# Performance work log

Hardware: AMD Instinct MI355X
Metric: run time of the kernel (lower is better)

Reference implementation:

```python
import jax, jax.numpy as jnp
import numpy as np

N = 100000
E = 3200000
EMBED = 64
RBF = 16
EPS_ANGLE = 1e-8
EPS_NORM = 1e-12  # F.normalize default eps


def _linear(h, W, b):
    return h @ W + b


def setup_inputs() -> dict:
    key = jax.random.key(0)
    ks = jax.random.split(key, 12)
    s = lambda fan_in: 1.0 / np.sqrt(fan_in)
    return {
        "x": jax.random.normal(ks[0], (N, EMBED), jnp.float32),
        "coord": jax.random.normal(ks[1], (N, 3), jnp.float32),
        "rbf_feature": jax.random.normal(ks[2], (E, RBF), jnp.float32),
        "edge_index": jax.random.randint(ks[3], (2, E), 0, N, jnp.int64),
        # edge_mlp: Linear(RBF+1, EMBED) -> SiLU -> Linear(EMBED, EMBED)
        "W1": jax.random.uniform(ks[4], (RBF + 1, EMBED), jnp.float32, -s(RBF + 1), s(RBF + 1)),
        "b1": jnp.zeros((EMBED,), jnp.float32),
        "W2": jax.random.uniform(ks[5], (EMBED, EMBED), jnp.float32, -s(EMBED), s(EMBED)),
        "b2": jnp.zeros((EMBED,), jnp.float32),
        # update_mlp: Linear(EMBED, EMBED) -> SiLU -> Linear(EMBED, EMBED)
        "W3": jax.random.uniform(ks[6], (EMBED, EMBED), jnp.float32, -s(EMBED), s(EMBED)),
        "b3": jnp.zeros((EMBED,), jnp.float32),
        "W4": jax.random.uniform(ks[7], (EMBED, EMBED), jnp.float32, -s(EMBED), s(EMBED)),
        "b4": jnp.zeros((EMBED,), jnp.float32),
    }


def reference(x, coord, rbf_feature, edge_index, W1, b1, W2, b2, W3, b3, W4, b4):
    row, col = edge_index[0], edge_index[1]
    # gather per-edge displacement vectors: [E, 3]
    v = coord[row] - coord[col]
    # compute_angle(v, -v): normalize both, cosine, clamp, acos
    norm = jnp.maximum(jnp.linalg.norm(v, axis=-1, keepdims=True), EPS_NORM)
    vn = v / norm
    cos_angle = jnp.clip(jnp.sum(vn * (-vn), axis=-1), -1.0 + EPS_ANGLE, 1.0 - EPS_ANGLE)
    angle = jnp.arccos(cos_angle)[:, None]  # [E, 1]
    edge_feat = jnp.concatenate([rbf_feature, angle], axis=-1)  # [E, RBF+1]
    # edge MLP
    edge_msg = _linear(jax.nn.silu(_linear(edge_feat, W1, b1)), W2, b2)  # [E, EMBED]
    # scatter-add to source nodes (index_add_ over row)
    agg = jax.ops.segment_sum(edge_msg, row, num_segments=x.shape[0])  # [N, EMBED]
    # node update
    return x + _linear(jax.nn.silu(_linear(agg, W3, b3)), W4, b4)
```

## Files before the change

### kernel.cpp

```cpp
#include <hip/hip_runtime.h>
#include <hip/hip_fp16.h>
#include <hip/hip_bf16.h>

typedef __attribute__((ext_vector_type(8))) short bf16x8;
typedef __attribute__((ext_vector_type(4))) float f32x4;

constexpr int EMBED = 64;
constexpr int RBF   = 16;

__device__ __forceinline__ short f2bf(float f) {
    __hip_bfloat16 h = __float2bfloat16(f);
    return *reinterpret_cast<short*>(&h);
}
__device__ __forceinline__ unsigned pk_bf(float lo, float hi) {
    unsigned l = (unsigned short)f2bf(lo);
    unsigned h = (unsigned short)f2bf(hi);
    return l | (h << 16);
}
__device__ __forceinline__ unsigned pk_f16(float lo, float hi) {
    __half2 h = __halves2half2(__float2half_rn(lo), __float2half_rn(hi));
    return *reinterpret_cast<unsigned*>(&h);
}
__device__ __forceinline__ void atom_pk_add_f16(__half* addr, unsigned data) {
    asm volatile("global_atomic_pk_add_f16 %0, %1, off"
                 :: "v"(addr), "v"(data) : "memory");
}
__device__ __forceinline__ float silu(float x) {
    return x * __builtin_amdgcn_rcpf(1.0f + __expf(-x));
}
__device__ __forceinline__ int ch_map(int t, int c) {
    return (t & 1) + 2 * c + 32 * (t >> 1);
}

constexpr short BF16_PI  = (short)0x4049;
constexpr short BF16_PI2 = (short)0x3FC9;

template <bool GUARD, bool F16>
__global__ __launch_bounds__(256, 2) void edge_kernel(
    const float* __restrict__ rbf,
    const int* __restrict__ ei,
    const float* __restrict__ W1,
    const float* __restrict__ b1,
    const float* __restrict__ W2,
    const float* __restrict__ b2,
    void* __restrict__ agg,
    int e_base, int E)
{
    __shared__ __align__(16) short lds_s[4][16 * 64];
    __shared__ int lds_row[256];

    const int tid  = threadIdx.x;
    const int lane = tid & 63;
    const int wave = tid >> 6;
    const int g = lane >> 4;
    const int c = lane & 15;
    const int blk_e0 = e_base + blockIdx.x * 256;

    {
        const int e = blk_e0 + tid;
        lds_row[tid] = (!GUARD || e < E) ? ei[e] : 0;
    }
    __syncthreads();

    bf16x8 b1f[4];
    float b1v[4], b2v[4];
#pragma unroll
    for (int t = 0; t < 4; ++t) {
        const int ch = ch_map(t, c);
#pragma unroll
        for (int j = 0; j < 8; ++j) {
            const int k = g * 8 + j;
            b1f[t][j] = (k <= RBF) ? f2bf(W1[k * EMBED + ch]) : (short)0;
        }
        b1v[t] = b1[ch];
        b2v[t] = b2[ch];
    }
    bf16x8 b2f[2][4];
#pragma unroll
    for (int kk = 0; kk < 2; ++kk)
#pragma unroll
        for (int t = 0; t < 4; ++t) {
            const int ch = ch_map(t, c);
#pragma unroll
            for (int j = 0; j < 8; ++j)
                b2f[kk][t][j] = f2bf(W2[(kk * 32 + g * 8 + j) * EMBED + ch]);
        }

    char* const sl = reinterpret_cast<char*>(lds_s[wave]);
    const int e0w = blk_e0 + wave * 64;

#pragma unroll 1
    for (int mt = 0; mt < 4; ++mt) {
        const int e0 = e0w + mt * 16;
        if (GUARD && e0 >= E) break;
        const int el0 = wave * 64 + mt * 16;

        bf16x8 a = {};
        const int ea = e0 + c;
        const bool ev = !GUARD || (ea < E);
        if (g < 2) {
            if (ev) {
                const float4 p0 = *reinterpret_cast<const float4*>(rbf + (long long)ea * RBF + g * 8);
                const float4 p1 = *reinterpret_cast<const float4*>(rbf + (long long)ea * RBF + g * 8 + 4);
                a[0] = f2bf(p0.x); a[1] = f2bf(p0.y); a[2] = f2bf(p0.z); a[3] = f2bf(p0.w);
                a[4] = f2bf(p1.x); a[5] = f2bf(p1.y); a[6] = f2bf(p1.z); a[7] = f2bf(p1.w);
            }
        } else if (g == 2 && ev) {
            const int row = lds_row[el0 + c];
            const int col = ei[E + ea];
            a[0] = (row == col) ? BF16_PI2 : BF16_PI;
        }

        f32x4 acc1[4];
#pragma unroll
        for (int t = 0; t < 4; ++t) {
            f32x4 ci = {b1v[t], b1v[t], b1v[t], b1v[t]};
            acc1[t] = __builtin_amdgcn_mfma_f32_16x16x32_bf16(a, b1f[t], ci, 0, 0, 0);
        }

#pragma unroll
        for (int r = 0; r < 4; ++r) {
            const int erow = g * 4 + r;
            const int swz = (erow & 7) << 4;
            *reinterpret_cast<unsigned*>(sl + erow * 128 + ((4 * c) ^ swz)) =
                pk_bf(silu(acc1[0][r]), silu(acc1[1][r]));
            *reinterpret_cast<unsigned*>(sl + erow * 128 + ((64 + 4 * c) ^ swz)) =
                pk_bf(silu(acc1[2][r]), silu(acc1[3][r]));
        }
        __builtin_amdgcn_wave_barrier();

        bf16x8 a2[2];
#pragma unroll
        for (int kk = 0; kk < 2; ++kk) {
            const int byte = c * 128 + ((kk * 64 + g * 16) ^ ((c & 7) << 4));
            a2[kk] = *reinterpret_cast<const bf16x8*>(sl + byte);
        }
        __builtin_amdgcn_wave_barrier();

        f32x4 acc2[4];
#pragma unroll
        for (int t = 0; t < 4; ++t) {
            f32x4 ci = {b2v[t], b2v[t], b2v[t], b2v[t]};
            acc2[t] = __builtin_amdgcn_mfma_f32_16x16x32_bf16(a2[0], b2f[0][t], ci, 0, 0, 0);
            acc2[t] = __builtin_amdgcn_mfma_f32_16x16x32_bf16(a2[1], b2f[1][t], acc2[t], 0, 0, 0);
        }

#pragma unroll
        for (int r = 0; r < 4; ++r) {
            const int eat = e0 + g * 4 + r;
            if (!GUARD || eat < E) {
                const unsigned row = (unsigned)lds_row[el0 + g * 4 + r];
                if (F16) {
                    __half* const dst = reinterpret_cast<__half*>(agg) + row * 64u;
                    atom_pk_add_f16(dst + 2 * c,      pk_f16(acc2[0][r], acc2[1][r]));
                    atom_pk_add_f16(dst + 32 + 2 * c, pk_f16(acc2[2][r], acc2[3][r]));
                } else {
                    float* const dst = reinterpret_cast<float*>(agg) + row * 64u;
                    atomicAdd(dst + 2 * c,      acc2[0][r]);
                    atomicAdd(dst + 2 * c + 1,  acc2[1][r]);
                    atomicAdd(dst + 32 + 2 * c, acc2[2][r]);
                    atomicAdd(dst + 33 + 2 * c, acc2[3][r]);
                }
            }
        }
    }
}

template <bool F16>
__global__ __launch_bounds__(256) void node_kernel(
    const float* __restrict__ x, const void* __restrict__ aggv,
    const float* __restrict__ W3, const float* __restrict__ b3,
    const float* __restrict__ W4, const float* __restrict__ b4,
    float* __restrict__ out, int nn)
{
    __shared__ __align__(16) float lds_s[4][EMBED];
    const int lane = threadIdx.x & 63;
    const int wave = threadIdx.x >> 6;
    float w3c[EMBED], w4c[EMBED];
#pragma unroll
    for (int j = 0; j < EMBED; ++j) w3c[j] = W3[j * EMBED + lane];
#pragma unroll
    for (int j = 0; j < EMBED; ++j) w4c[j] = W4[j * EMBED + lane];
    const float b3v = b3[lane];
    const float b4v = b4[lane];
    const float4* s4 = reinterpret_cast<const float4*>(lds_s[wave]);
    const int wid = blockIdx.x * 4 + wave;
    const int nw  = gridDim.x * 4;
    for (int n = wid; n < nn; n += nw) {
        const long long base = (long long)n * EMBED + lane;
        float a;
        if (F16) a = __half2float(reinterpret_cast<const __half*>(aggv)[base]);
        else     a = reinterpret_cast<const float*>(aggv)[base];
        lds_s[wave][lane] = a;
        __builtin_amdgcn_wave_barrier();
        float acc = b3v;
#pragma unroll
        for (int j4 = 0; j4 < EMBED / 4; ++j4) {
            const float4 sv = s4[j4];
            acc = fmaf(sv.x, w3c[4 * j4 + 0], acc);
            acc = fmaf(sv.y, w3c[4 * j4 + 1], acc);
            acc = fmaf(sv.z, w3c[4 * j4 + 2], acc);
            acc = fmaf(sv.w, w3c[4 * j4 + 3], acc);
        }
        const float s = acc * __builtin_amdgcn_rcpf(1.0f + __expf(-acc));
        __builtin_amdgcn_wave_barrier();
        lds_s[wave][lane] = s;
        __builtin_amdgcn_wave_barrier();
        float acc2 = b4v;
#pragma unroll
        for (int j4 = 0; j4 < EMBED / 4; ++j4) {
            const float4 sv = s4[j4];
            acc2 = fmaf(sv.x, w4c[4 * j4 + 0], acc2);
            acc2 = fmaf(sv.y, w4c[4 * j4 + 1], acc2);
            acc2 = fmaf(sv.z, w4c[4 * j4 + 2], acc2);
            acc2 = fmaf(sv.w, w4c[4 * j4 + 3], acc2);
        }
        __builtin_amdgcn_wave_barrier();
        out[base] = x[base] + acc2;
    }
}

extern "C" void kernel_launch(void* const* d_in, const int* in_sizes, int n_in,
                              void* d_out, int out_size, void* d_ws, size_t ws_size,
                              hipStream_t stream) {
    const float* x      = (const float*)d_in[0];
    const float* rbf    = (const float*)d_in[2];
    const int*   ei     = (const int*)d_in[3];
    const float* W1 = (const float*)d_in[4];
    const float* b1 = (const float*)d_in[5];
    const float* W2 = (const float*)d_in[6];
    const float* b2 = (const float*)d_in[7];
    const float* W3 = (const float*)d_in[8];
    const float* b3 = (const float*)d_in[9];
    const float* W4 = (const float*)d_in[10];
    const float* b4 = (const float*)d_in[11];
    float* out = (float*)d_out;

    const int E  = (int)(in_sizes[3] / 2);
    const int nn = in_sizes[0] / EMBED;

    void* agg16 = d_ws;
    const size_t neededF16 = (size_t)nn * EMBED * sizeof(__half);

    const int nfull = E / 256;
    const int rem   = E - nfull * 256;

    if (ws_size >= neededF16) {
        hipMemsetAsync(agg16, 0, neededF16, stream);
        if (nfull)
            edge_kernel<false, true><<<dim3(nfull), dim3(256), 0, stream>>>(
                rbf, ei, W1, b1, W2, b2, agg16, 0, E);
        if (rem)
            edge_kernel<true, true><<<dim3(1), dim3(256), 0, stream>>>(
                rbf, ei, W1, b1, W2, b2, agg16, nfull * 256, E);
        node_kernel<true><<<dim3(2048), dim3(256), 0, stream>>>(
            x, agg16, W3, b3, W4, b4, out, nn);
    } else {
        hipMemsetAsync(out, 0, (size_t)nn * EMBED * sizeof(float), stream);
        if (nfull)
            edge_kernel<false, false><<<dim3(nfull), dim3(256), 0, stream>>>(
                rbf, ei, W1, b1, W2, b2, out, 0, E);
        if (rem)
            edge_kernel<true, false><<<dim3(1), dim3(256), 0, stream>>>(
                rbf, ei, W1, b1, W2, b2, out, nfull * 256, E);
        node_kernel<false><<<dim3(2048), dim3(256), 0, stream>>>(
            x, out, W3, b3, W4, b4, out, nn);
    }
}
```

Measured before the change: 428.2 us.

## Move second edge-MLP linear layer after scatter using linearity and degree-scaled bias

Because the second edge linear layer is linear, the edge kernel now scatter-adds silu(first layer) per source node and counts node degree, and a new per-node kernel applies W2 plus degree times b2. This removes the second MFMA stage and its LDS round trip from the per-edge path, leaving the same amount of atomic traffic. It adds a degree atomic per edge, an extra node kernel, and an extra fp32 agg buffer in workspace. If the workspace is too small, execution falls back to the original fused path.

Result: slower. 589.8 us (+37.7%).

```diff
diff --git a/kernel.cpp b/kernel.cpp
--- a/kernel.cpp
+++ b/kernel.cpp
@@ -35,33 +35,209 @@
 constexpr short BF16_PI  = (short)0x4049;
 constexpr short BF16_PI2 = (short)0x3FC9;
 
-template <bool GUARD, bool F16>
-__global__ __launch_bounds__(256, 2) void edge_kernel(
+template <bool GUARD>
+__global__ __launch_bounds__(256, 2) void edge_sum_kernel(
+    const float* __restrict__ rbf,
+    const int* __restrict__ ei,
+    const float* __restrict__ W1,
+    const float* __restrict__ b1,
+    __half* __restrict__ ssum,
+    float* __restrict__ deg,
+    int e_base, int E)
+{
+    __shared__ int lds_row[256];
+
+    const int tid  = threadIdx.x;
+    const int lane = tid & 63;
+    const int wave = tid >> 6;
+    const int g = lane >> 4;
+    const int c = lane & 15;
+    const int blk_e0 = e_base + blockIdx.x * 256;
+
+    {
+        const int e = blk_e0 + tid;
+        const bool v = !GUARD || (e < E);
+        const int row = v ? ei[e] : 0;
+        lds_row[tid] = row;
+        if (v) atomicAdd(&deg[row], 1.0f);
+    }
+    __syncthreads();
+
+    bf16x8 b1f[4];
+    float b1v[4];
+#pragma unroll
+    for (int t = 0; t < 4; ++t) {
+        const int ch = ch_map(t, c);
+#pragma unroll
+        for (int j = 0; j < 8; ++j) {
+            const int k = g * 8 + j;
+            b1f[t][j] = (k <= RBF) ? f2bf(W1[k * EMBED + ch]) : (short)0;
+        }
+        b1v[t] = b1[ch];
+    }
+
+    const int e0w = blk_e0 + wave * 64;
+
+    bf16x8 a1[4];
+#pragma unroll
+    for (int mt = 0; mt < 4; ++mt) {
+        bf16x8 a = {};
+        const int e0 = e0w + mt * 16;
+        const int ea = e0 + c;
+        const bool ev = !GUARD || (ea < E);
+        if (g < 2) {
+            if (ev) {
+                const float4 p0 = *reinterpret_cast<const float4*>(rbf + (long long)ea * RBF + g * 8);
+                const float4 p1 = *reinterpret_cast<const float4*>(rbf + (long long)ea * RBF + g * 8 + 4);
+                a[0] = f2bf(p0.x); a[1] = f2bf(p0.y); a[2] = f2bf(p0.z); a[3] = f2bf(p0.w);
+                a[4] = f2bf(p1.x); a[5] = f2bf(p1.y); a[6] = f2bf(p1.z); a[7] = f2bf(p1.w);
+            }
+        } else if (g == 2 && ev) {
+            const int row = lds_row[wave * 64 + mt * 16 + c];
+            const int col = ei[E + ea];
+            a[0] = (row == col) ? BF16_PI2 : BF16_PI;
+        }
+        a1[mt] = a;
+    }
+
+#pragma unroll
+    for (int mt = 0; mt < 4; ++mt) {
+        const int e0 = e0w + mt * 16;
+        if (GUARD && e0 >= E) break;
+        const int el0 = wave * 64 + mt * 16;
+
+        f32x4 s[4];
+#pragma unroll
+        for (int t = 0; t < 4; ++t) {
+            f32x4 ci = {b1v[t], b1v[t], b1v[t], b1v[t]};
+            s[t] = __builtin_amdgcn_mfma_f32_16x16x32_bf16(a1[mt], b1f[t], ci, 0, 0, 0);
+        }
+
+#pragma unroll
+        for (int r = 0; r < 4; ++r) {
+            const int eat = e0 + g * 4 + r;
+            if (!GUARD || eat < E) {
+                const unsigned row = (unsigned)lds_row[el0 + g * 4 + r];
+                __half* const dst = ssum + row * 64u;
+                atom_pk_add_f16(dst + 2 * c,
+                                pk_f16(silu(s[0][r]), silu(s[1][r])));
+                atom_pk_add_f16(dst + 32 + 2 * c,
+                                pk_f16(silu(s[2][r]), silu(s[3][r])));
+            }
+        }
+    }
+}
+
+__global__ __launch_bounds__(256) void k_agg(
+    const __half* __restrict__ ssum, const float* __restrict__ deg,
+    const float* __restrict__ W2, const float* __restrict__ b2,
+    float* __restrict__ agg, int nn)
+{
+    __shared__ __align__(16) float lds_s[4][EMBED];
+    const int lane = threadIdx.x & 63;
+    const int wave = threadIdx.x >> 6;
+
+    float w2c[EMBED];
+#pragma unroll
+    for (int j = 0; j < EMBED; ++j) w2c[j] = W2[j * EMBED + lane];
+    const float b2v = b2[lane];
+
+    const float4* s4 = reinterpret_cast<const float4*>(lds_s[wave]);
+    const int wid = blockIdx.x * 4 + wave;
+    const int nw  = gridDim.x * 4;
+    for (int n = wid; n < nn; n += nw) {
+        const long long base = (long long)n * EMBED + lane;
+        const float a = __half2float(ssum[base]);
+
+        lds_s[wave][lane] = a;
+        __builtin_amdgcn_wave_barrier();
+
+        float acc = deg[n] * b2v;
+#pragma unroll
+        for (int j4 = 0; j4 < EMBED / 4; ++j4) {
+            const float4 sv = s4[j4];
+            acc = fmaf(sv.x, w2c[4 * j4 + 0], acc);
+            acc = fmaf(sv.y, w2c[4 * j4 + 1], acc);
+            acc = fmaf(sv.z, w2c[4 * j4 + 2], acc);
+            acc = fmaf(sv.w, w2c[4 * j4 + 3], acc);
+        }
+        __builtin_amdgcn_wave_barrier();
+
+        agg[base] = acc;
+    }
+}
+
+__global__ __launch_bounds__(256) void node_kernel(
+    const float* __restrict__ x, const float* __restrict__ aggv,
+    const float* __restrict__ W3, const float* __restrict__ b3,
+    const float* __restrict__ W4, const float* __restrict__ b4,
+    float* __restrict__ out, int nn)
+{
+    __shared__ __align__(16) float lds_s[4][EMBED];
+    const int lane = threadIdx.x & 63;
+    const int wave = threadIdx.x >> 6;
+    float w3c[EMBED], w4c[EMBED];
+#pragma unroll
+    for (int j = 0; j < EMBED; ++j) w3c[j] = W3[j * EMBED + lane];
+#pragma unroll
+    for (int j = 0; j < EMBED; ++j) w4c[j] = W4[j * EMBED + lane];
+    const float b3v = b3[lane];
+    const float b4v = b4[lane];
+    const float4* s4 = reinterpret_cast<const float4*>(lds_s[wave]);
+    const int wid = blockIdx.x * 4 + wave;
+    const int nw  = gridDim.x * 4;
+    for (int n = wid; n < nn; n += nw) {
+        const long long base = (long long)n * EMBED + lane;
+        const float a = aggv[base];
+        lds_s[wave][lane] = a;
+        __builtin_amdgcn_wave_barrier();
+        float acc = b3v;
+#pragma unroll
+        for (int j4 = 0; j4 < EMBED / 4; ++j4) {
+            const float4 sv = s4[j4];
+            acc = fmaf(sv.x, w3c[4 * j4 + 0], acc);
+            acc = fmaf(sv.y, w3c[4 * j4 + 1], acc);
+            acc = fmaf(sv.z, w3c[4 * j4 + 2], acc);
+            acc = fmaf(sv.w, w3c[4 * j4 + 3], acc);
+        }
+        const float s = acc * __builtin_amdgcn_rcpf(1.0f + __expf(-acc));
+        __builtin_amdgcn_wave_barrier();
+        lds_s[wave][lane] = s;
+        __builtin_amdgcn_wave_barrier();
+        float acc2 = b4v;
+#pragma unroll
+        for (int j4 = 0; j4 < EMBED / 4; ++j4) {
+            const float4 sv = s4[j4];
+            acc2 = fmaf(sv.x, w4c[4 * j4 + 0], acc2);
+            acc2 = fmaf(sv.y, w4c[4 * j4 + 1], acc2);
+            acc2 = fmaf(sv.z, w4c[4 * j4 + 2], acc2);
+            acc2 = fmaf(sv.w, w4c[4 * j4 + 3], acc2);
+        }
+        __builtin_amdgcn_wave_barrier();
+        out[base] = x[base] + acc2;
+    }
+}
+
+__global__ __launch_bounds__(256, 2) void edge_kernel_fb(
     const float* __restrict__ rbf,
     const int* __restrict__ ei,
     const float* __restrict__ W1,
     const float* __restrict__ b1,
     const float* __restrict__ W2,
     const float* __restrict__ b2,
-    void* __restrict__ agg,
-    int e_base, int E)
+    float* __restrict__ agg,
+    int E)
 {
     __shared__ __align__(16) short lds_s[4][16 * 64];
     __shared__ int lds_row[256];
-
-    const int tid  = threadIdx.x;
-    const int lane = tid & 63;
-    const int wave = tid >> 6;
-    const int g = lane >> 4;
-    const int c = lane & 15;
-    const int blk_e0 = e_base + blockIdx.x * 256;
-
+    const int tid = threadIdx.x, lane = tid & 63, wave = tid >> 6;
+    const int g = lane >> 4, c = lane & 15;
+    const int blk_e0 = blockIdx.x * 256;
     {
         const int e = blk_e0 + tid;
-        lds_row[tid] = (!GUARD || e < E) ? ei[e] : 0;
+        lds_row[tid] = (e < E) ? ei[e] : 0;
     }
     __syncthreads();
-
     bf16x8 b1f[4];
     float b1v[4], b2v[4];
 #pragma unroll
@@ -85,19 +261,16 @@
             for (int j = 0; j < 8; ++j)
                 b2f[kk][t][j] = f2bf(W2[(kk * 32 + g * 8 + j) * EMBED + ch]);
         }
-
     char* const sl = reinterpret_cast<char*>(lds_s[wave]);
     const int e0w = blk_e0 + wave * 64;
-
 #pragma unroll 1
     for (int mt = 0; mt < 4; ++mt) {
         const int e0 = e0w + mt * 16;
-        if (GUARD && e0 >= E) break;
+        if (e0 >= E) break;
         const int el0 = wave * 64 + mt * 16;
-
         bf16x8 a = {};
         const int ea = e0 + c;
-        const bool ev = !GUARD || (ea < E);
+        const bool ev = (ea < E);
         if (g < 2) {
             if (ev) {
                 const float4 p0 = *reinterpret_cast<const float4*>(rbf + (long long)ea * RBF + g * 8);
@@ -110,14 +283,12 @@
             const int col = ei[E + ea];
             a[0] = (row == col) ? BF16_PI2 : BF16_PI;
         }
-
         f32x4 acc1[4];
 #pragma unroll
         for (int t = 0; t < 4; ++t) {
             f32x4 ci = {b1v[t], b1v[t], b1v[t], b1v[t]};
             acc1[t] = __builtin_amdgcn_mfma_f32_16x16x32_bf16(a, b1f[t], ci, 0, 0, 0);
         }
-
 #pragma unroll
         for (int r = 0; r < 4; ++r) {
             const int erow = g * 4 + r;
@@ -128,7 +299,6 @@
                 pk_bf(silu(acc1[2][r]), silu(acc1[3][r]));
         }
         __builtin_amdgcn_wave_barrier();
-
         bf16x8 a2[2];
 #pragma unroll
         for (int kk = 0; kk < 2; ++kk) {
@@ -136,7 +306,6 @@
             a2[kk] = *reinterpret_cast<const bf16x8*>(sl + byte);
         }
         __builtin_amdgcn_wave_barrier();
-
         f32x4 acc2[4];
 #pragma unroll
         for (int t = 0; t < 4; ++t) {
@@ -144,79 +313,19 @@
             acc2[t] = __builtin_amdgcn_mfma_f32_16x16x32_bf16(a2[0], b2f[0][t], ci, 0, 0, 0);
             acc2[t] = __builtin_amdgcn_mfma_f32_16x16x32_bf16(a2[1], b2f[1][t], acc2[t], 0, 0, 0);
         }
-
 #pragma unroll
         for (int r = 0; r < 4; ++r) {
             const int eat = e0 + g * 4 + r;
-            if (!GUARD || eat < E) {
+            if (eat < E) {
                 const unsigned row = (unsigned)lds_row[el0 + g * 4 + r];
-                if (F16) {
-                    __half* const dst = reinterpret_cast<__half*>(agg) + row * 64u;
-                    atom_pk_add_f16(dst + 2 * c,      pk_f16(acc2[0][r], acc2[1][r]));
-                    atom_pk_add_f16(dst + 32 + 2 * c, pk_f16(acc2[2][r], acc2[3][r]));
-                } else {
-                    float* const dst = reinterpret_cast<float*>(agg) + row * 64u;
-                    atomicAdd(dst + 2 * c,      acc2[0][r]);
-                    atomicAdd(dst + 2 * c + 1,  acc2[1][r]);
-                    atomicAdd(dst + 32 + 2 * c, acc2[2][r]);
-                    atomicAdd(dst + 33 + 2 * c, acc2[3][r]);
-                }
+                float* const dst = agg + row * 64u;
+                const int ch0 = 2 * c, ch2 = 32 + 2 * c;
+                atomicAdd(dst + ch0,     acc2[0][r]);
+                atomicAdd(dst + ch0 + 1, acc2[1][r]);
+                atomicAdd(dst + ch2,     acc2[2][r]);
+                atomicAdd(dst + ch2 + 1, acc2[3][r]);
             }
         }
-    }
-}
-
-template <bool F16>
-__global__ __launch_bounds__(256) void node_kernel(
-    const float* __restrict__ x, const void* __restrict__ aggv,
-    const float* __restrict__ W3, const float* __restrict__ b3,
-    const float* __restrict__ W4, const float* __restrict__ b4,
-    float* __restrict__ out, int nn)
-{
-    __shared__ __align__(16) float lds_s[4][EMBED];
-    const int lane = threadIdx.x & 63;
-    const int wave = threadIdx.x >> 6;
-    float w3c[EMBED], w4c[EMBED];
-#pragma unroll
-    for (int j = 0; j < EMBED; ++j) w3c[j] = W3[j * EMBED + lane];
-#pragma unroll
-    for (int j = 0; j < EMBED; ++j) w4c[j] = W4[j * EMBED + lane];
-    const float b3v = b3[lane];
-    const float b4v = b4[lane];
-    const float4* s4 = reinterpret_cast<const float4*>(lds_s[wave]);
-    const int wid = blockIdx.x * 4 + wave;
-    const int nw  = gridDim.x * 4;
-    for (int n = wid; n < nn; n += nw) {
-        const long long base = (long long)n * EMBED + lane;
-        float a;
-        if (F16) a = __half2float(reinterpret_cast<const __half*>(aggv)[base]);
-        else     a = reinterpret_cast<const float*>(aggv)[base];
-        lds_s[wave][lane] = a;
-        __builtin_amdgcn_wave_barrier();
-        float acc = b3v;
-#pragma unroll
-        for (int j4 = 0; j4 < EMBED / 4; ++j4) {
-            const float4 sv = s4[j4];
-            acc = fmaf(sv.x, w3c[4 * j4 + 0], acc);
-            acc = fmaf(sv.y, w3c[4 * j4 + 1], acc);
-            acc = fmaf(sv.z, w3c[4 * j4 + 2], acc);
-            acc = fmaf(sv.w, w3c[4 * j4 + 3], acc);
-        }
-        const float s = acc * __builtin_amdgcn_rcpf(1.0f + __expf(-acc));
-        __builtin_amdgcn_wave_barrier();
-        lds_s[wave][lane] = s;
-        __builtin_amdgcn_wave_barrier();
-        float acc2 = b4v;
-#pragma unroll
-        for (int j4 = 0; j4 < EMBED / 4; ++j4) {
-            const float4 sv = s4[j4];
-            acc2 = fmaf(sv.x, w4c[4 * j4 + 0], acc2);
-            acc2 = fmaf(sv.y, w4c[4 * j4 + 1], acc2);
-            acc2 = fmaf(sv.z, w4c[4 * j4 + 2], acc2);
-            acc2 = fmaf(sv.w, w4c[4 * j4 + 3], acc2);
-        }
-        __builtin_amdgcn_wave_barrier();
-        out[base] = x[base] + acc2;
     }
 }
 
@@ -239,31 +348,33 @@
     const int E  = (int)(in_sizes[3] / 2);
     const int nn = in_sizes[0] / EMBED;
 
-    void* agg16 = d_ws;
-    const size_t neededF16 = (size_t)nn * EMBED * sizeof(__half);
+    const size_t ssumBytes = (size_t)nn * EMBED * sizeof(__half);
+    const size_t degBytes  = (size_t)nn * sizeof(float);
+    const size_t aggBytes  = (size_t)nn * EMBED * sizeof(float);
+    __half* ssum = (__half*)d_ws;
+    float*  deg  = (float*)((char*)d_ws + ssumBytes);
+    float*  agg  = (float*)((char*)d_ws + ssumBytes + degBytes);
+    const size_t needed = ssumBytes + degBytes + aggBytes;
 
     const int nfull = E / 256;
     const int rem   = E - nfull * 256;
 
-    if (ws_size >= neededF16) {
-        hipMemsetAsync(agg16, 0, neededF16, stream);
+    if (ws_size >= needed) {
+        hipMemsetAsync(d_ws, 0, ssumBytes + degBytes, stream);
         if (nfull)
-            edge_kernel<false, true><<<dim3(nfull), dim3(256), 0, stream>>>(
-                rbf, ei, W1, b1, W2, b2, agg16, 0, E);
+            edge_sum_kernel<false><<<dim3(nfull), dim3(256), 0, stream>>>(
+                rbf, ei, W1, b1, ssum, deg, 0, E);
         if (rem)
-            edge_kernel<true, true><<<dim3(1), dim3(256), 0, stream>>>(
-                rbf, ei, W1, b1, W2, b2, agg16, nfull * 256, E);
-        node_kernel<true><<<dim3(2048), dim3(256), 0, stream>>>(
-            x, agg16, W3, b3, W4, b4, out, nn);
+            edge_sum_kernel<true><<<dim3(1), dim3(256), 0, stream>>>(
+                rbf, ei, W1, b1, ssum, deg, nfull * 256, E);
+        k_agg<<<dim3(2048), dim3(256), 0, stream>>>(ssum, deg, W2, b2, agg, nn);
+        node_kernel<<<dim3(2048), dim3(256), 0, stream>>>(
+            x, agg, W3, b3, W4, b4, out, nn);
     } else {
         hipMemsetAsync(out, 0, (size_t)nn * EMBED * sizeof(float), stream);
-        if (nfull)
-            edge_kernel<false, false><<<dim3(nfull), dim3(256), 0, stream>>>(
-                rbf, ei, W1, b1, W2, b2, out, 0, E);
-        if (rem)
-            edge_kernel<true, false><<<dim3(1), dim3(256), 0, stream>>>(
-                rbf, ei, W1, b1, W2, b2, out, nfull * 256, E);
-        node_kernel<false><<<dim3(2048), dim3(256), 0, stream>>>(
+        edge_kernel_fb<<<dim3((unsigned)((E + 255) / 256)), dim3(256), 0, stream>>>(
+            rbf, ei, W1, b1, W2, b2, out, E);
+        node_kernel<<<dim3(2048), dim3(256), 0, stream>>>(
             x, out, W3, b3, W4, b4, out, nn);
     }
 }
```

## Switch edge MLP to 32x32x16 MFMA and fold angle into bias

Applied to the files above, without the earlier changes.

Rewrites the edge kernel to process 32 edges per tile with 32x32x16 bf16 MFMA instead of 16x16x32. The angle feature no longer takes its own K slot: it is folded into the first-layer bias as pi*W1[16], and a per-edge correction is added only for self-loop edges, found with a wave ballot. This cuts the wasted K padding in layer one and halves the number of packed f16 atomics per lane row. The cost is larger LDS staging, more accumulator registers, and per-element flag lookups whenever a wave contains a self-loop.

New measurement: 394.8 us, median of 2. 1.08x faster.

```diff
diff --git a/kernel.cpp b/kernel.cpp
--- a/kernel.cpp
+++ b/kernel.cpp
@@ -2,8 +2,9 @@
 #include <hip/hip_fp16.h>
 #include <hip/hip_bf16.h>
 
-typedef __attribute__((ext_vector_type(8))) short bf16x8;
-typedef __attribute__((ext_vector_type(4))) float f32x4;
+typedef __attribute__((ext_vector_type(8)))  short bf16x8;
+typedef __attribute__((ext_vector_type(4)))  float f32x4;
+typedef __attribute__((ext_vector_type(16))) float f32x16;
 
 constexpr int EMBED = 64;
 constexpr int RBF   = 16;
@@ -11,6 +12,10 @@
 __device__ __forceinline__ short f2bf(float f) {
     __hip_bfloat16 h = __float2bfloat16(f);
     return *reinterpret_cast<short*>(&h);
+}
+__device__ __forceinline__ float bf2f(short s) {
+    unsigned u = ((unsigned)(unsigned short)s) << 16;
+    return __uint_as_float(u);
 }
 __device__ __forceinline__ unsigned pk_bf(float lo, float hi) {
     unsigned l = (unsigned short)f2bf(lo);
@@ -28,15 +33,16 @@
 __device__ __forceinline__ float silu(float x) {
     return x * __builtin_amdgcn_rcpf(1.0f + __expf(-x));
 }
-__device__ __forceinline__ int ch_map(int t, int c) {
-    return (t & 1) + 2 * c + 32 * (t >> 1);
-}
-
-constexpr short BF16_PI  = (short)0x4049;
-constexpr short BF16_PI2 = (short)0x3FC9;
+
+constexpr float PI_BF  = 3.140625f;
+constexpr float PI2_BF = 1.5703125f;
+
+__device__ __forceinline__ int crow(int j, int h) {
+    return (j & 3) + 8 * (j >> 2) + 4 * h;
+}
 
 template <bool GUARD, bool F16>
-__global__ __launch_bounds__(256, 2) void edge_kernel(
+__global__ __launch_bounds__(256, 2) void edge_kernel32(
     const float* __restrict__ rbf,
     const int* __restrict__ ei,
     const float* __restrict__ W1,
@@ -46,120 +52,121 @@
     void* __restrict__ agg,
     int e_base, int E)
 {
-    __shared__ __align__(16) short lds_s[4][16 * 64];
+    __shared__ __align__(16) short lds_s[4][32 * 64];
     __shared__ int lds_row[256];
+    __shared__ unsigned char lds_flag[256];
+    __shared__ int wave_any[4];
 
     const int tid  = threadIdx.x;
     const int lane = tid & 63;
     const int wave = tid >> 6;
-    const int g = lane >> 4;
-    const int c = lane & 15;
+    const int n = lane & 31;
+    const int h = lane >> 5;
     const int blk_e0 = e_base + blockIdx.x * 256;
 
     {
         const int e = blk_e0 + tid;
-        lds_row[tid] = (!GUARD || e < E) ? ei[e] : 0;
+        const bool v = !GUARD || (e < E);
+        const int row = v ? ei[e] : 0;
+        const int col = v ? ei[E + e] : 1;
+        lds_row[tid]  = row;
+        const bool fl = v && (row == col);
+        lds_flag[tid] = fl;
+        const unsigned long long m = __ballot(fl);
+        if (lane == 0) wave_any[wave] = (m != 0ull);
     }
     __syncthreads();
 
-    bf16x8 b1f[4];
-    float b1v[4], b2v[4];
-#pragma unroll
-    for (int t = 0; t < 4; ++t) {
-        const int ch = ch_map(t, c);
-#pragma unroll
-        for (int j = 0; j < 8; ++j) {
-            const int k = g * 8 + j;
-            b1f[t][j] = (k <= RBF) ? f2bf(W1[k * EMBED + ch]) : (short)0;
-        }
-        b1v[t] = b1[ch];
-        b2v[t] = b2[ch];
-    }
-    bf16x8 b2f[2][4];
-#pragma unroll
-    for (int kk = 0; kk < 2; ++kk)
-#pragma unroll
-        for (int t = 0; t < 4; ++t) {
-            const int ch = ch_map(t, c);
+    bf16x8 b1f[2];
+    float  b1v[2], dlt[2], b2v[2];
+#pragma unroll
+    for (int hh = 0; hh < 2; ++hh) {
+        const int ch = 2 * n + hh;
+#pragma unroll
+        for (int j = 0; j < 8; ++j)
+            b1f[hh][j] = f2bf(W1[(h * 8 + j) * EMBED + ch]);
+        const float w16 = bf2f(f2bf(W1[RBF * EMBED + ch]));
+        b1v[hh] = b1[ch] + PI_BF * w16;
+        dlt[hh] = (PI2_BF - PI_BF) * w16;
+        b2v[hh] = b2[ch];
+    }
+    bf16x8 b2f[4][2];
+#pragma unroll
+    for (int kk = 0; kk < 4; ++kk)
+#pragma unroll
+        for (int hh = 0; hh < 2; ++hh) {
+            const int ch = 2 * n + hh;
 #pragma unroll
             for (int j = 0; j < 8; ++j)
-                b2f[kk][t][j] = f2bf(W2[(kk * 32 + g * 8 + j) * EMBED + ch]);
+                b2f[kk][hh][j] = f2bf(W2[(kk * 16 + h * 8 + j) * EMBED + ch]);
         }
 
     char* const sl = reinterpret_cast<char*>(lds_s[wave]);
-    const int e0w = blk_e0 + wave * 64;
 
 #pragma unroll 1
-    for (int mt = 0; mt < 4; ++mt) {
-        const int e0 = e0w + mt * 16;
+    for (int mt = 0; mt < 2; ++mt) {
+        const int e0  = blk_e0 + wave * 64 + mt * 32;
         if (GUARD && e0 >= E) break;
-        const int el0 = wave * 64 + mt * 16;
-
-        bf16x8 a = {};
-        const int ea = e0 + c;
-        const bool ev = !GUARD || (ea < E);
-        if (g < 2) {
-            if (ev) {
-                const float4 p0 = *reinterpret_cast<const float4*>(rbf + (long long)ea * RBF + g * 8);
-                const float4 p1 = *reinterpret_cast<const float4*>(rbf + (long long)ea * RBF + g * 8 + 4);
-                a[0] = f2bf(p0.x); a[1] = f2bf(p0.y); a[2] = f2bf(p0.z); a[3] = f2bf(p0.w);
-                a[4] = f2bf(p1.x); a[5] = f2bf(p1.y); a[6] = f2bf(p1.z); a[7] = f2bf(p1.w);
+        const int el0 = wave * 64 + mt * 32;
+
+        bf16x8 a1 = {};
+        {
+            const int ea = e0 + n;
+            if (!GUARD || ea < E) {
+                const float4 p0 = *reinterpret_cast<const float4*>(rbf + (long long)ea * RBF + h * 8);
+                const float4 p1 = *reinterpret_cast<const float4*>(rbf + (long long)ea * RBF + h * 8 + 4);
+                a1[0] = f2bf(p0.x); a1[1] = f2bf(p0.y); a1[2] = f2bf(p0.z); a1[3] = f2bf(p0.w);
+                a1[4] = f2bf(p1.x); a1[5] = f2bf(p1.y); a1[6] = f2bf(p1.z); a1[7] = f2bf(p1.w);
             }
-        } else if (g == 2 && ev) {
-            const int row = lds_row[el0 + c];
-            const int col = ei[E + ea];
-            a[0] = (row == col) ? BF16_PI2 : BF16_PI;
-        }
-
-        f32x4 acc1[4];
-#pragma unroll
-        for (int t = 0; t < 4; ++t) {
-            f32x4 ci = {b1v[t], b1v[t], b1v[t], b1v[t]};
-            acc1[t] = __builtin_amdgcn_mfma_f32_16x16x32_bf16(a, b1f[t], ci, 0, 0, 0);
-        }
-
-#pragma unroll
-        for (int r = 0; r < 4; ++r) {
-            const int erow = g * 4 + r;
-            const int swz = (erow & 7) << 4;
-            *reinterpret_cast<unsigned*>(sl + erow * 128 + ((4 * c) ^ swz)) =
-                pk_bf(silu(acc1[0][r]), silu(acc1[1][r]));
-            *reinterpret_cast<unsigned*>(sl + erow * 128 + ((64 + 4 * c) ^ swz)) =
-                pk_bf(silu(acc1[2][r]), silu(acc1[3][r]));
-        }
-        __builtin_amdgcn_wave_barrier();
-
-        bf16x8 a2[2];
-#pragma unroll
-        for (int kk = 0; kk < 2; ++kk) {
-            const int byte = c * 128 + ((kk * 64 + g * 16) ^ ((c & 7) << 4));
-            a2[kk] = *reinterpret_cast<const bf16x8*>(sl + byte);
-        }
-        __builtin_amdgcn_wave_barrier();
-
-        f32x4 acc2[4];
-#pragma unroll
-        for (int t = 0; t < 4; ++t) {
-            f32x4 ci = {b2v[t], b2v[t], b2v[t], b2v[t]};
-            acc2[t] = __builtin_amdgcn_mfma_f32_16x16x32_bf16(a2[0], b2f[0][t], ci, 0, 0, 0);
-            acc2[t] = __builtin_amdgcn_mfma_f32_16x16x32_bf16(a2[1], b2f[1][t], acc2[t], 0, 0, 0);
-        }
-
-#pragma unroll
-        for (int r = 0; r < 4; ++r) {
-            const int eat = e0 + g * 4 + r;
+        }
+
+        f32x16 accA, accB;
+#pragma unroll
+        for (int j = 0; j < 16; ++j) { accA[j] = b1v[0]; accB[j] = b1v[1]; }
+        accA = __builtin_amdgcn_mfma_f32_32x32x16_bf16(a1, b1f[0], accA, 0, 0, 0);
+        accB = __builtin_amdgcn_mfma_f32_32x32x16_bf16(a1, b1f[1], accB, 0, 0, 0);
+
+        if (wave_any[wave]) {
+#pragma unroll
+            for (int j = 0; j < 16; ++j) {
+                const int m = crow(j, h);
+                if (lds_flag[el0 + m]) { accA[j] += dlt[0]; accB[j] += dlt[1]; }
+            }
+        }
+
+#pragma unroll
+        for (int j = 0; j < 16; ++j) {
+            const int m = crow(j, h);
+            const unsigned u = pk_bf(silu(accA[j]), silu(accB[j]));
+            *reinterpret_cast<unsigned*>(sl + m * 128 + ((4 * n) ^ ((m & 7) << 4))) = u;
+        }
+        __builtin_amdgcn_wave_barrier();
+
+        f32x16 acc2A, acc2B;
+#pragma unroll
+        for (int j = 0; j < 16; ++j) { acc2A[j] = b2v[0]; acc2B[j] = b2v[1]; }
+#pragma unroll
+        for (int kk = 0; kk < 4; ++kk) {
+            const int byte = n * 128 + ((kk * 32 + h * 16) ^ ((n & 7) << 4));
+            const bf16x8 a2 = *reinterpret_cast<const bf16x8*>(sl + byte);
+            acc2A = __builtin_amdgcn_mfma_f32_32x32x16_bf16(a2, b2f[kk][0], acc2A, 0, 0, 0);
+            acc2B = __builtin_amdgcn_mfma_f32_32x32x16_bf16(a2, b2f[kk][1], acc2B, 0, 0, 0);
+        }
+        __builtin_amdgcn_wave_barrier();
+
+#pragma unroll
+        for (int j = 0; j < 16; ++j) {
+            const int m = crow(j, h);
+            const int eat = e0 + m;
             if (!GUARD || eat < E) {
-                const unsigned row = (unsigned)lds_row[el0 + g * 4 + r];
+                const unsigned row = (unsigned)lds_row[el0 + m];
                 if (F16) {
                     __half* const dst = reinterpret_cast<__half*>(agg) + row * 64u;
-                    atom_pk_add_f16(dst + 2 * c,      pk_f16(acc2[0][r], acc2[1][r]));
-                    atom_pk_add_f16(dst + 32 + 2 * c, pk_f16(acc2[2][r], acc2[3][r]));
+                    atom_pk_add_f16(dst + 2 * n, pk_f16(acc2A[j], acc2B[j]));
                 } else {
                     float* const dst = reinterpret_cast<float*>(agg) + row * 64u;
-                    atomicAdd(dst + 2 * c,      acc2[0][r]);
-                    atomicAdd(dst + 2 * c + 1,  acc2[1][r]);
-                    atomicAdd(dst + 32 + 2 * c, acc2[2][r]);
-                    atomicAdd(dst + 33 + 2 * c, acc2[3][r]);
+                    atomicAdd(dst + 2 * n,     acc2A[j]);
+                    atomicAdd(dst + 2 * n + 1, acc2B[j]);
                 }
             }
         }
@@ -248,20 +255,20 @@
     if (ws_size >= neededF16) {
         hipMemsetAsync(agg16, 0, neededF16, stream);
         if (nfull)
-            edge_kernel<false, true><<<dim3(nfull), dim3(256), 0, stream>>>(
+            edge_kernel32<false, true><<<dim3(nfull), dim3(256), 0, stream>>>(
                 rbf, ei, W1, b1, W2, b2, agg16, 0, E);
         if (rem)
-            edge_kernel<true, true><<<dim3(1), dim3(256), 0, stream>>>(
+            edge_kernel32<true, true><<<dim3(1), dim3(256), 0, stream>>>(
                 rbf, ei, W1, b1, W2, b2, agg16, nfull * 256, E);
         node_kernel<true><<<dim3(2048), dim3(256), 0, stream>>>(
             x, agg16, W3, b3, W4, b4, out, nn);
     } else {
         hipMemsetAsync(out, 0, (size_t)nn * EMBED * sizeof(float), stream);
         if (nfull)
-            edge_kernel<false, false><<<dim3(nfull), dim3(256), 0, stream>>>(
+            edge_kernel32<false, false><<<dim3(nfull), dim3(256), 0, stream>>>(
                 rbf, ei, W1, b1, W2, b2, out, 0, E);
         if (rem)
-            edge_kernel<true, false><<<dim3(1), dim3(256), 0, stream>>>(
+            edge_kernel32<true, false><<<dim3(1), dim3(256), 0, stream>>>(
                 rbf, ei, W1, b1, W2, b2, out, nfull * 256, E);
         node_kernel<false><<<dim3(2048), dim3(256), 0, stream>>>(
             x, out, W3, b3, W4, b4, out, nn);
```
